# Performance work log

Measured on AMD Instinct MI355X. Metric: run time of the kernel, lower is better.

The kernel has to match this reference:

```python
import jax, jax.numpy as jnp
import numpy as np
from jax import lax

DIMS, IN_DIM, NW = 32, 32, 8
N, T, H, W = 8, 16, 112, 112
EPS = 1e-5

def setup_inputs() -> dict:
    key = jax.random.key(0)
    ks = jax.random.split(key, 12)
    fan = IN_DIM * 27
    inp = {
        'x': jax.random.normal(ks[0], (N, IN_DIM, T, H, W), jnp.float32),
        'std_x': jax.random.normal(ks[1], (N, 1, 32, 32), jnp.float32),
        'epochs_num': 5,
        'weights': jax.random.normal(ks[2], (NW, DIMS, IN_DIM, 3, 3, 3), jnp.float32) * np.sqrt(2.0 / fan),
        'biases': jax.random.normal(ks[3], (NW, DIMS), jnp.float32),
        'conv1_w': jax.random.normal(ks[4], (16, 1, 5, 5), jnp.float32) * 0.2,
        'conv1_b': jax.random.normal(ks[5], (16,), jnp.float32) * 0.1,
        'conv2_w': jax.random.normal(ks[6], (32, 16, 5, 5), jnp.float32) * 0.05,
        'conv2_b': jax.random.normal(ks[7], (32,), jnp.float32) * 0.1,
        'fc_w': jax.random.normal(ks[8], (NW, 32), jnp.float32) * 0.1,
        'fc_b': jax.random.normal(ks[9], (NW,), jnp.float32) * 0.1,
        'bn_gamma': jnp.ones((DIMS,), jnp.float32),
        'bn_beta': jnp.zeros((DIMS,), jnp.float32),
    }
    return inp

def _routing(std_x, c1w, c1b, c2w, c2b, fcw, fcb, tau):
    dn = ('NCHW', 'OIHW', 'NCHW')
    h = lax.conv_general_dilated(std_x, c1w, (1, 1), 'VALID', dimension_numbers=dn)
    h = jax.nn.relu(h + c1b[None, :, None, None])
    h = lax.conv_general_dilated(h, c2w, (1, 1), 'VALID', dimension_numbers=dn)
    h = jax.nn.relu(h + c2b[None, :, None, None])
    h = jnp.max(h, axis=(2, 3))                      # adaptive max pool to 1 -> [n,32]
    logits = h @ fcw.T + fcb                          # [n, num_weights]
    return jax.nn.softmax(logits / tau, axis=1)

def reference(x, std_x, epochs_num, weights, biases, conv1_w, conv1_b, conv2_w, conv2_b, fc_w, fc_b, bn_gamma, bn_beta):
    tau = 30.0 - 2.9 * epochs_num if epochs_num < 10 else 1.0
    phi = _routing(std_x, conv1_w, conv1_b, conv2_w, conv2_b, fc_w, fc_b, tau)
    dyn_w = jnp.einsum('bn,ncidhw->bcidhw', phi, weights)   # per-sample filters [n,dims,in,3,3,3]
    dyn_b = jnp.einsum('bn,nc->bc', phi, biases)            # [n,dims]
    dn3 = ('NCDHW', 'OIDHW', 'NCDHW')
    def per_sample(xi, wi):
        return lax.conv_general_dilated(xi[None], wi, (1, 1, 1), 'SAME', dimension_numbers=dn3)[0]
    y = jax.vmap(per_sample)(x, dyn_w)                      # [n,dims,T,H,W]
    y = y + dyn_b[:, :, None, None, None]
    # BatchNorm3d (training mode: batch stats, biased variance)
    mean = jnp.mean(y, axis=(0, 2, 3, 4))
    var = jnp.var(y, axis=(0, 2, 3, 4))
    y = (y - mean[None, :, None, None, None]) * lax.rsqrt(var + EPS)[None, :, None, None, None]
    y = y * bn_gamma[None, :, None, None, None] + bn_beta[None, :, None, None, None]
    return jax.nn.relu(y)
```

## Files before the change

### kernel.cpp

```cpp
#include <hip/hip_runtime.h>
#include <hip/hip_bf16.h>

#define IN_DIM 32
#define DIMS   32
#define NW     8
#define NB     8
#define TT     16
#define HH     112
#define WW     112
#define HW     (HH*WW)
#define CHW    (TT*HW)
#define EPS    1e-5f

typedef __attribute__((ext_vector_type(8))) short bf16x8;
typedef __attribute__((ext_vector_type(4))) float f32x4;

static __device__ __forceinline__ unsigned short f2bf(float f) {
    unsigned u = __float_as_uint(f);
    unsigned r = u + 0x7FFFu + ((u >> 16) & 1u);
    return (unsigned short)(r >> 16);
}

static __device__ __forceinline__ void gload_lds16(const void* gptr, void* lptr) {
    __builtin_amdgcn_global_load_lds(
        (const __attribute__((address_space(1))) unsigned int*)gptr,
        (__attribute__((address_space(3))) unsigned int*)lptr,
        16, 0, 0);
}

#define WSF_PHI    0
#define WSF_DYNB   64
#define WSF_STATS  320
#define WSF_ZERO   384
#define WSF_HDR_FLOATS 448
#define XT_USHORTS  ((size_t)NB*CHW*32)
#define WS_NEED_BYTES (WSF_HDR_FLOATS*4 + (size_t)NB*27*1024*2 + XT_USHORTS*2)

#define WS_PHI    0
#define WS_DYNW   64
#define WS_DYNB   221248
#define WS_STATS  221504
#define WS_SS     221568

__global__ __launch_bounds__(256)
void routing_conv1_kernel(const float* __restrict__ std_x,
                          const float* __restrict__ c1w, const float* __restrict__ c1b,
                          float* __restrict__ h1g)
{
    const int oc = blockIdx.x, b = blockIdx.y;
    const int tid = threadIdx.x;
    __shared__ float sx[1024];
    for (int i = tid; i < 1024; i += 256) sx[i] = std_x[b * 1024 + i];
    __syncthreads();

    float wloc[25];
    #pragma unroll
    for (int k = 0; k < 25; ++k) wloc[k] = c1w[oc * 25 + k];
    const float bias = c1b[oc];

    for (int idx = tid; idx < 784; idx += 256) {
        int xw = idx % 28, xh = idx / 28;
        float s = bias;
        #pragma unroll
        for (int ky = 0; ky < 5; ++ky)
            #pragma unroll
            for (int kx = 0; kx < 5; ++kx)
                s = fmaf(sx[(xh + ky) * 32 + xw + kx], wloc[ky * 5 + kx], s);
        h1g[(b * 16 + oc) * 784 + idx] = fmaxf(s, 0.f);
    }
}

__global__ __launch_bounds__(256)
void routing_conv2max_kernel(const float* __restrict__ h1g,
                             const float* __restrict__ c2w, const float* __restrict__ c2b,
                             float* __restrict__ cmax)
{
    const int oc = blockIdx.x, b = blockIdx.y;
    const int tid = threadIdx.x;
    __shared__ float h1s[16 * 784];
    __shared__ float wred[4];

    for (int i = tid; i < 16 * 784; i += 256) h1s[i] = h1g[b * (16 * 784) + i];
    __syncthreads();

    float m = 0.f;
    for (int idx = tid; idx < 576; idx += 256) {
        int xw = idx % 24, xh = idx / 24;
        float s = c2b[oc];
        for (int ic = 0; ic < 16; ++ic) {
            const float* hp = &h1s[ic * 784];
            const float* wp = &c2w[(oc * 16 + ic) * 25];
            #pragma unroll
            for (int ky = 0; ky < 5; ++ky)
                #pragma unroll
                for (int kx = 0; kx < 5; ++kx)
                    s = fmaf(hp[(xh + ky) * 28 + xw + kx], wp[ky * 5 + kx], s);
        }
        m = fmaxf(m, s);
    }
    #pragma unroll
    for (int off = 32; off >= 1; off >>= 1) m = fmaxf(m, __shfl_down(m, off));
    if ((tid & 63) == 0) wred[tid >> 6] = m;
    __syncthreads();
    if (tid == 0) {
        float r = fmaxf(fmaxf(wred[0], wred[1]), fmaxf(wred[2], wred[3]));
        cmax[b * 32 + oc] = r;
    }
}

__global__ __launch_bounds__(64)
void routing_fc_kernel(const float* __restrict__ cmax, const int* __restrict__ epochs,
                       const float* __restrict__ fcw, const float* __restrict__ fcb,
                       float* __restrict__ phi_out)
{
    const int tid = threadIdx.x;
    const int b = tid >> 3, n = tid & 7;
    int ep = epochs[0];
    float tau = (ep < 10) ? (30.0f - 2.9f * (float)ep) : 1.0f;
    float s = fcb[n];
    #pragma unroll
    for (int k = 0; k < 32; ++k) s = fmaf(cmax[b * 32 + k], fcw[n * 32 + k], s);
    s /= tau;
    float mx = s;
    #pragma unroll
    for (int off = 1; off < 8; off <<= 1) mx = fmaxf(mx, __shfl_xor(mx, off, 8));
    float e = expf(s - mx);
    float den = e;
    #pragma unroll
    for (int off = 1; off < 8; off <<= 1) den += __shfl_xor(den, off, 8);
    phi_out[b * 8 + n] = e / den;
}

#define XS 232
__global__ __launch_bounds__(256)
void xpose_kernel(const float* __restrict__ x, unsigned short* __restrict__ xT)
{
    const int h = blockIdx.x, t = blockIdx.y, b = blockIdx.z;
    const int tid = threadIdx.x;
    __shared__ __align__(16) unsigned char lds[32 * XS];

    for (int idx = tid; idx < 32 * 28; idx += 256) {
        int ic = idx / 28;
        int w4 = idx - ic * 28;
        const float4 v = *(const float4*)(x + (((size_t)(b * 32 + ic) * TT + t) * HW) + h * 112 + w4 * 4);
        uint2 pk;
        pk.x = (unsigned)f2bf(v.x) | ((unsigned)f2bf(v.y) << 16);
        pk.y = (unsigned)f2bf(v.z) | ((unsigned)f2bf(v.w) << 16);
        *(uint2*)(lds + ic * XS + w4 * 8) = pk;
    }
    __syncthreads();

    unsigned short* op = xT + ((((size_t)b * TT + t) * HH + h) * WW) * 32;
    for (int idx = tid; idx < 448; idx += 256) {
        int w = idx >> 2, icg = idx & 3;
        unsigned int pk[4];
        #pragma unroll
        for (int j = 0; j < 4; ++j) {
            unsigned short lo = *(unsigned short*)(lds + (icg * 8 + 2 * j) * XS + w * 2);
            unsigned short hi = *(unsigned short*)(lds + (icg * 8 + 2 * j + 1) * XS + w * 2);
            pk[j] = (unsigned int)lo | ((unsigned int)hi << 16);
        }
        uint4 v; v.x = pk[0]; v.y = pk[1]; v.z = pk[2]; v.w = pk[3];
        *(uint4*)(op + (size_t)w * 32 + icg * 8) = v;
    }
}

__global__ __launch_bounds__(256)
void dynwb_kernel(const float* __restrict__ phi, const float* __restrict__ weights,
                  const float* __restrict__ biases, unsigned short* __restrict__ dwb,
                  float* __restrict__ dyn_b, float* __restrict__ statszero)
{
    const int oc = blockIdx.x;
    const int b  = blockIdx.y;
    const int tid = threadIdx.x;
    __shared__ float ph[8];
    if (tid < 8) ph[tid] = phi[b * 8 + tid];
    __syncthreads();

    for (int i = tid; i < 864; i += 256) {
        float s = 0.f;
        #pragma unroll
        for (int n = 0; n < 8; ++n)
            s = fmaf(ph[n], weights[(size_t)(n * 32 + oc) * 864 + i], s);
        int ic = i / 27;
        int tap = i - 27 * ic;
        dwb[((size_t)(b * 27 + tap) << 10) + (oc << 5) + ic] = f2bf(s);
    }
    if (tid == 0) {
        float s = 0.f;
        #pragma unroll
        for (int n = 0; n < 8; ++n) s = fmaf(ph[n], biases[n * 32 + oc], s);
        dyn_b[b * 32 + oc] = s;
    }
    if (oc == 0 && b == 0 && tid < 128) statszero[tid] = 0.f;
}

#define XROWSTRIDE   1152
#define XLDS_BYTES   20736
#define WLDS_BYTES   55296
#define PLANE_BYTES_G 802816ull
__global__ __launch_bounds__(256, 2)
void convmf_kernel(const unsigned short* __restrict__ xT, const unsigned short* __restrict__ dwb,
                   const float* __restrict__ dyn_b, float* __restrict__ y,
                   float* __restrict__ stats)
{
    const int hblk = blockIdx.x / 7, wblk = blockIdx.x % 7;
    const int tpair = blockIdx.y, b = blockIdx.z;
    const int h0 = hblk * 16, w0 = wblk * 16, t0 = tpair * 2;
    const int tid = threadIdx.x;
    const int lane = tid & 63, wv = tid >> 6;
    const int l15 = lane & 15, lg = lane >> 4;

    __shared__ __align__(16) unsigned char wlds[WLDS_BYTES];
    __shared__ __align__(16) unsigned char xlds[XLDS_BYTES];
    __shared__ float sred[4][64];

    {
        const unsigned short* wb = dwb + (size_t)b * 27 * 1024;
        unsigned char* ldsw = wlds + (size_t)(tid & ~63) * 16;
        #pragma unroll
        for (int k = 0; k < 14; ++k) {
            if (k < 13 || tid < 128) {
                int cid = k * 256 + tid;
                int tap = cid >> 7;
                int rem = cid & 127;
                int oc  = rem >> 2;
                int icg_s = rem & 3;
                int icg_l = icg_s ^ ((oc >> 1) & 3);
                gload_lds16(wb + tap * 1024 + oc * 32 + icg_l * 8, ldsw + k * 4096);
            }
        }
    }

    const unsigned char* xbase = (const unsigned char*)xT + (size_t)b * TT * PLANE_BYTES_G;
    int srcoff[6], dsto[6];
    bool okj[6], valid[6];
    #pragma unroll
    for (int j = 0; j < 6; ++j) {
        int cid = j * 256 + tid;
        int hr = cid / 72, rem = cid - hr * 72;
        int p = rem >> 2, icg = rem & 3;
        int gh = h0 - 1 + hr, gw = w0 - 1 + p;
        valid[j] = (cid < 1296);
        okj[j] = valid[j] && ((unsigned)gh < (unsigned)HH) && ((unsigned)gw < (unsigned)WW);
        srcoff[j] = (gh * WW + gw) * 64 + icg * 16;
        dsto[j] = (hr * 72 + p * 4 + (icg ^ ((p >> 1) & 3))) * 16;
    }
    uint4 xs[6];

#define LOADX(TX) do {                                                        \
        const int tx_ = (TX);                                                 \
        const bool tok_ = ((unsigned)tx_ < (unsigned)TT);                     \
        const unsigned char* pb_ = xbase + (size_t)tx_ * PLANE_BYTES_G;       \
        _Pragma("unroll")                                                     \
        for (int j = 0; j < 6; ++j) {                                         \
            uint4 v_; v_.x = 0; v_.y = 0; v_.z = 0; v_.w = 0;                 \
            if (tok_ && okj[j]) v_ = *(const uint4*)(pb_ + srcoff[j]);        \
            xs[j] = v_;                                                       \
        }                                                                     \
    } while (0)

#define WRITEX() do {                                                         \
        _Pragma("unroll")                                                     \
        for (int j = 0; j < 6; ++j)                                           \
            if (valid[j]) *(uint4*)(xlds + dsto[j]) = xs[j];                  \
    } while (0)

    const int wsw = l15 * 64 + ((lg ^ ((l15 >> 1) & 3)) * 16);
    int xoff[3];
    #pragma unroll
    for (int dw = 0; dw < 3; ++dw) {
        int px = l15 + dw;
        xoff[dw] = px * 64 + ((lg ^ ((px >> 1) & 3)) * 16);
    }

    f32x4 acc0[4][2], acc1[4][2];
    #pragma unroll
    for (int g = 0; g < 4; ++g)
        #pragma unroll
        for (int M = 0; M < 2; ++M) { acc0[g][M] = (f32x4)0.f; acc1[g][M] = (f32x4)0.f; }

    LOADX(t0 - 1);
    asm volatile("s_waitcnt vmcnt(0)" ::: "memory");
    WRITEX();
    __syncthreads();

    #pragma unroll
    for (int tp = 0; tp < 4; ++tp) {
        if (tp < 3) LOADX(t0 + tp);

        const bool do0 = (tp <= 2), do1 = (tp >= 1);
        #pragma unroll
        for (int dhw = 0; dhw < 9; ++dhw) {
            const int dh = dhw / 3, dw = dhw - dh * 3;
            bf16x8 a00, a01, a10, a11;
            if (do0) {
                const int off = (tp * 9 + dhw) * 2048 + wsw;
                a00 = *(const bf16x8*)(wlds + off);
                a01 = *(const bf16x8*)(wlds + off + 1024);
            }
            if (do1) {
                const int off = ((tp - 1) * 9 + dhw) * 2048 + wsw;
                a10 = *(const bf16x8*)(wlds + off);
                a11 = *(const bf16x8*)(wlds + off + 1024);
            }
            const int rb = wv * 4 + dh;
            #pragma unroll
            for (int g = 0; g < 4; ++g) {
                bf16x8 bb = *(const bf16x8*)(xlds + (rb + g) * XROWSTRIDE + xoff[dw]);
                if (do0) {
                    acc0[g][0] = __builtin_amdgcn_mfma_f32_16x16x32_bf16(a00, bb, acc0[g][0], 0, 0, 0);
                    acc0[g][1] = __builtin_amdgcn_mfma_f32_16x16x32_bf16(a01, bb, acc0[g][1], 0, 0, 0);
                }
                if (do1) {
                    acc1[g][0] = __builtin_amdgcn_mfma_f32_16x16x32_bf16(a10, bb, acc1[g][0], 0, 0, 0);
                    acc1[g][1] = __builtin_amdgcn_mfma_f32_16x16x32_bf16(a11, bb, acc1[g][1], 0, 0, 0);
                }
            }
        }

        if (tp < 3) {
            __syncthreads();
            asm volatile("s_waitcnt vmcnt(0)" ::: "memory");
            WRITEX();
            __syncthreads();
        }
    }
#undef LOADX
#undef WRITEX

    f32x4 bias[2];
    #pragma unroll
    for (int M = 0; M < 2; ++M)
        #pragma unroll
        for (int r = 0; r < 4; ++r)
            bias[M][r] = dyn_b[b * 32 + 16 * M + lg * 4 + r];

    float sumv[2][4], sqv[2][4];
    #pragma unroll
    for (int M = 0; M < 2; ++M)
        #pragma unroll
        for (int r = 0; r < 4; ++r) { sumv[M][r] = 0.f; sqv[M][r] = 0.f; }

    #pragma unroll
    for (int g = 0; g < 4; ++g) {
        const int h = h0 + wv * 4 + g;
        #pragma unroll
        for (int M = 0; M < 2; ++M) {
            f32x4 v0 = acc0[g][M] + bias[M];
            f32x4 v1 = acc1[g][M] + bias[M];
            const int oc0 = 16 * M + lg * 4;
            size_t base = (((size_t)(b * 32 + oc0) * TT + t0) * HW) + h * 112 + w0 + l15;
            #pragma unroll
            for (int r = 0; r < 4; ++r) {
                sumv[M][r] += v0[r] + v1[r];
                sqv[M][r]  += v0[r] * v0[r] + v1[r] * v1[r];
                y[base + (size_t)r * TT * HW] = v0[r];
                y[base + (size_t)r * TT * HW + HW] = v1[r];
            }
        }
    }

    #pragma unroll
    for (int off = 1; off < 16; off <<= 1) {
        #pragma unroll
        for (int M = 0; M < 2; ++M)
            #pragma unroll
            for (int r = 0; r < 4; ++r) {
                sumv[M][r] += __shfl_xor(sumv[M][r], off);
                sqv[M][r]  += __shfl_xor(sqv[M][r], off);
            }
    }
    if (l15 == 0) {
        #pragma unroll
        for (int M = 0; M < 2; ++M)
            #pragma unroll
            for (int r = 0; r < 4; ++r) {
                int ch = 16 * M + lg * 4 + r;
                sred[wv][ch] = sumv[M][r];
                sred[wv][32 + ch] = sqv[M][r];
            }
    }
    __syncthreads();
    if (tid < 64) {
        float v = sred[0][tid] + sred[1][tid] + sred[2][tid] + sred[3][tid];
        atomicAdd(&stats[tid], v);
    }
}

__global__ __launch_bounds__(256)
void norm_relu_fused_kernel(float* __restrict__ y, const float* __restrict__ stats,
                            const float* __restrict__ gamma, const float* __restrict__ beta)
{
    __shared__ float ssc[32], ssh[32];
    if (threadIdx.x < 32) {
        int c = threadIdx.x;
        const float M = (float)NB * (float)CHW;
        float mean = stats[c] / M;
        float var  = stats[32 + c] / M - mean * mean;
        float sc = gamma[c] * rsqrtf(var + EPS);
        ssc[c] = sc;
        ssh[c] = beta[c] - mean * sc;
    }
    __syncthreads();

    const long long total4 = (long long)NB * DIMS * CHW / 4;
    const int nthreads = gridDim.x * blockDim.x;
    float4* y4 = reinterpret_cast<float4*>(y);
    for (long long i = (long long)blockIdx.x * blockDim.x + threadIdx.x; i < total4; i += nthreads) {
        int c = (int)((i / (CHW / 4)) & 31);
        float sc = ssc[c];
        float sh = ssh[c];
        float4 v = y4[i];
        v.x = fmaxf(fmaf(v.x, sc, sh), 0.f);
        v.y = fmaxf(fmaf(v.y, sc, sh), 0.f);
        v.z = fmaxf(fmaf(v.z, sc, sh), 0.f);
        v.w = fmaxf(fmaf(v.w, sc, sh), 0.f);
        y4[i] = v;
    }
}

__global__ __launch_bounds__(256)
void routing_kernel(const float* __restrict__ std_x, const int* __restrict__ epochs,
                    const float* __restrict__ c1w, const float* __restrict__ c1b,
                    const float* __restrict__ c2w, const float* __restrict__ c2b,
                    const float* __restrict__ fcw, const float* __restrict__ fcb,
                    float* __restrict__ phi_out)
{
    const int b = blockIdx.x;
    const int tid = threadIdx.x;
    __shared__ float sx[32 * 32];
    __shared__ float h1[16 * 28 * 28];
    __shared__ float cmax[32];

    for (int i = tid; i < 1024; i += 256) sx[i] = std_x[b * 1024 + i];
    if (tid < 32) cmax[tid] = 0.f;
    __syncthreads();

    for (int idx = tid; idx < 16 * 28 * 28; idx += 256) {
        int xw = idx % 28;
        int r = idx / 28;
        int xh = r % 28;
        int oc = r / 28;
        float s = c1b[oc];
        #pragma unroll
        for (int ky = 0; ky < 5; ++ky)
            #pragma unroll
            for (int kx = 0; kx < 5; ++kx)
                s = fmaf(sx[(xh + ky) * 32 + xw + kx], c1w[oc * 25 + ky * 5 + kx], s);
        h1[idx] = fmaxf(s, 0.f);
    }
    __syncthreads();

    for (int idx = tid; idx < 32 * 24 * 24; idx += 256) {
        int xw = idx % 24;
        int r = idx / 24;
        int xh = r % 24;
        int oc = r / 24;
        float s = c2b[oc];
        for (int ic = 0; ic < 16; ++ic) {
            const float* hp = &h1[ic * 784];
            const float* wp = &c2w[(oc * 16 + ic) * 25];
            #pragma unroll
            for (int ky = 0; ky < 5; ++ky)
                #pragma unroll
                for (int kx = 0; kx < 5; ++kx)
                    s = fmaf(hp[(xh + ky) * 28 + xw + kx], wp[ky * 5 + kx], s);
        }
        s = fmaxf(s, 0.f);
        atomicMax(reinterpret_cast<int*>(&cmax[oc]), __float_as_int(s));
    }
    __syncthreads();

    if (tid == 0) {
        int ep = epochs[0];
        float tau = (ep < 10) ? (30.0f - 2.9f * (float)ep) : 1.0f;
        float lg[8];
        float mx = -1e30f;
        #pragma unroll
        for (int n = 0; n < 8; ++n) {
            float s = fcb[n];
            #pragma unroll
            for (int k = 0; k < 32; ++k) s = fmaf(cmax[k], fcw[n * 32 + k], s);
            lg[n] = s / tau;
            mx = fmaxf(mx, lg[n]);
        }
        float den = 0.f;
        #pragma unroll
        for (int n = 0; n < 8; ++n) { lg[n] = expf(lg[n] - mx); den += lg[n]; }
        #pragma unroll
        for (int n = 0; n < 8; ++n) phi_out[b * 8 + n] = lg[n] / den;
    }
}

__global__ __launch_bounds__(256)
void dynw_kernel(const float* __restrict__ phi, const float* __restrict__ weights,
                 const float* __restrict__ biases, float* __restrict__ dyn_w,
                 float* __restrict__ dyn_b, float* __restrict__ stats)
{
    const int b = blockIdx.x;
    const int tid = threadIdx.x;
    __shared__ float ph[8];
    if (tid < 8) ph[tid] = phi[b * 8 + tid];
    __syncthreads();

    for (int j = tid; j < DIMS * IN_DIM * 27; j += 256) {
        float s = 0.f;
        #pragma unroll
        for (int n = 0; n < 8; ++n) s = fmaf(ph[n], weights[n * (DIMS * IN_DIM * 27) + j], s);
        dyn_w[b * (DIMS * IN_DIM * 27) + j] = s;
    }
    if (tid < 32) {
        float s = 0.f;
        #pragma unroll
        for (int n = 0; n < 8; ++n) s = fmaf(ph[n], biases[n * 32 + tid], s);
        dyn_b[b * 32 + tid] = s;
    }
    if (b == 0 && tid < 64) stats[tid] = 0.f;
}

__global__ __launch_bounds__(256)
void conv3d_kernel(const float* __restrict__ x, const float* __restrict__ dyn_w,
                   const float* __restrict__ dyn_b, float* __restrict__ y,
                   float* __restrict__ stats)
{
    const int htile = blockIdx.x;
    const int t     = blockIdx.y;
    const int b     = blockIdx.z;
    const int tid   = threadIdx.x;
    const int w     = tid & 127;
    const int hh    = tid >> 7;
    const int h0    = htile * 2;

    __shared__ float tile[3][8][4][114];

    float acc[32];
    #pragma unroll
    for (int c = 0; c < 32; ++c) acc[c] = 0.f;

    const float* wb = dyn_w + b * (DIMS * IN_DIM * 27);
    const float* xb = x + (size_t)b * IN_DIM * CHW;

    for (int ic0 = 0; ic0 < 32; ic0 += 8) {
        __syncthreads();
        for (int idx = tid; idx < 3 * 8 * 4 * 114; idx += 256) {
            int w_ = idx % 114;
            int r  = idx / 114;
            int h_ = r & 3;
            int r2 = r >> 2;
            int i_ = r2 & 7;
            int dt_ = r2 >> 3;
            int gt = t + dt_ - 1;
            int gh = h0 - 1 + h_;
            int gw = w_ - 1;
            float v = 0.f;
            if ((unsigned)gt < (unsigned)TT && (unsigned)gh < (unsigned)HH && (unsigned)gw < (unsigned)WW)
                v = xb[(size_t)((ic0 + i_) * TT + gt) * HW + gh * WW + gw];
            tile[dt_][i_][h_][w_] = v;
        }
        __syncthreads();

        if (w < WW) {
            for (int i = 0; i < 8; ++i) {
                #pragma unroll
                for (int dt = 0; dt < 3; ++dt) {
                    float xv[9];
                    #pragma unroll
                    for (int dh = 0; dh < 3; ++dh)
                        #pragma unroll
                        for (int dw = 0; dw < 3; ++dw)
                            xv[dh * 3 + dw] = tile[dt][i][hh + dh][w + dw];
                    const float* wp = wb + (ic0 + i) * 27 + dt * 9;
                    #pragma unroll
                    for (int c = 0; c < 32; ++c) {
                        const float* wc = wp + c * 864;
                        #pragma unroll
                        for (int k = 0; k < 9; ++k)
                            acc[c] = fmaf(xv[k], wc[k], acc[c]);
                    }
                }
            }
        }
    }

    const float* db = dyn_b + b * 32;
    if (w < WW) {
        #pragma unroll
        for (int c = 0; c < 32; ++c) acc[c] += db[c];
    }

    __shared__ float ssum[32], ssq[32];
    if (tid < 32) { ssum[tid] = 0.f; ssq[tid] = 0.f; }
    __syncthreads();
    #pragma unroll
    for (int c = 0; c < 32; ++c) {
        float s = (w < WW) ? acc[c] : 0.f;
        float q = s * s;
        #pragma unroll
        for (int off = 32; off >= 1; off >>= 1) {
            s += __shfl_down(s, off);
            q += __shfl_down(q, off);
        }
        if ((tid & 63) == 0) { atomicAdd(&ssum[c], s); atomicAdd(&ssq[c], q); }
    }
    __syncthreads();
    if (tid < 32) {
        atomicAdd(&stats[tid], ssum[tid]);
        atomicAdd(&stats[32 + tid], ssq[tid]);
    }

    if (w < WW) {
        size_t base = ((size_t)(b * 32) * TT + t) * HW + (size_t)(h0 + hh) * WW + w;
        #pragma unroll
        for (int c = 0; c < 32; ++c)
            y[base + (size_t)c * CHW] = acc[c];
    }
}

__global__ void stats_finalize_kernel(const float* __restrict__ stats,
                                      const float* __restrict__ gamma,
                                      const float* __restrict__ beta,
                                      float* __restrict__ scaleshift)
{
    int c = threadIdx.x;
    const float M = (float)NB * (float)CHW;
    float mean = stats[c] / M;
    float var  = stats[32 + c] / M - mean * mean;
    float sc = gamma[c] * rsqrtf(var + EPS);
    scaleshift[c] = sc;
    scaleshift[32 + c] = beta[c] - mean * sc;
}

__global__ __launch_bounds__(256)
void norm_relu_kernel(float* __restrict__ y, const float* __restrict__ scaleshift)
{
    const long long total4 = (long long)NB * DIMS * CHW / 4;
    const int nthreads = gridDim.x * blockDim.x;
    float4* y4 = reinterpret_cast<float4*>(y);
    for (long long i = (long long)blockIdx.x * blockDim.x + threadIdx.x; i < total4; i += nthreads) {
        int c = (int)((i / (CHW / 4)) & 31);
        float sc = scaleshift[c];
        float sh = scaleshift[32 + c];
        float4 v = y4[i];
        v.x = fmaxf(fmaf(v.x, sc, sh), 0.f);
        v.y = fmaxf(fmaf(v.y, sc, sh), 0.f);
        v.z = fmaxf(fmaf(v.z, sc, sh), 0.f);
        v.w = fmaxf(fmaf(v.w, sc, sh), 0.f);
        y4[i] = v;
    }
}

extern "C" void kernel_launch(void* const* d_in, const int* in_sizes, int n_in,
                              void* d_out, int out_size, void* d_ws, size_t ws_size,
                              hipStream_t stream)
{
    const float* x      = (const float*)d_in[0];
    const float* std_x  = (const float*)d_in[1];
    const int*   epochs = (const int*)d_in[2];
    const float* weights= (const float*)d_in[3];
    const float* biases = (const float*)d_in[4];
    const float* c1w    = (const float*)d_in[5];
    const float* c1b    = (const float*)d_in[6];
    const float* c2w    = (const float*)d_in[7];
    const float* c2b    = (const float*)d_in[8];
    const float* fcw    = (const float*)d_in[9];
    const float* fcb    = (const float*)d_in[10];
    const float* gamma  = (const float*)d_in[11];
    const float* beta   = (const float*)d_in[12];

    float* out = (float*)d_out;
    float* ws  = (float*)d_ws;

    if (ws_size >= WS_NEED_BYTES) {
        float* phi   = ws + WSF_PHI;
        float* dyn_b = ws + WSF_DYNB;
        float* stats = ws + WSF_STATS;
        unsigned short* dwb = (unsigned short*)(ws + WSF_HDR_FLOATS);
        unsigned short* xT  = dwb + (size_t)NB * 27 * 1024;
        float* h1g  = (float*)xT;
        float* cmax = h1g + NB * 16 * 784;

        routing_conv1_kernel<<<dim3(16, NB), 256, 0, stream>>>(std_x, c1w, c1b, h1g);
        routing_conv2max_kernel<<<dim3(32, NB), 256, 0, stream>>>(h1g, c2w, c2b, cmax);
        routing_fc_kernel<<<1, 64, 0, stream>>>(cmax, epochs, fcw, fcb, phi);
        dynwb_kernel<<<dim3(32, NB), 256, 0, stream>>>(phi, weights, biases, dwb, dyn_b, stats);
        xpose_kernel<<<dim3(HH, TT, NB), 256, 0, stream>>>(x, xT);
        convmf_kernel<<<dim3(49, 8, NB), 256, 0, stream>>>(xT, dwb, dyn_b, out, stats);
        norm_relu_fused_kernel<<<2048, 256, 0, stream>>>(out, stats, gamma, beta);
    } else {
        float* phi   = ws + WS_PHI;
        float* dyn_w = ws + WS_DYNW;
        float* dyn_b = ws + WS_DYNB;
        float* stats = ws + WS_STATS;
        float* ss    = ws + WS_SS;

        routing_kernel<<<NB, 256, 0, stream>>>(std_x, epochs, c1w, c1b, c2w, c2b, fcw, fcb, phi);
        dynw_kernel<<<NB, 256, 0, stream>>>(phi, weights, biases, dyn_w, dyn_b, stats);
        conv3d_kernel<<<dim3(HH / 2, TT, NB), 256, 0, stream>>>(x, dyn_w, dyn_b, out, stats);
        stats_finalize_kernel<<<1, 32, 0, stream>>>(stats, gamma, beta, ss);
        norm_relu_kernel<<<2048, 256, 0, stream>>>(out, ss);
    }
}
```

Before: 571.0 us.

## Fuse bf16 transpose into conv load and store conv output as bf16

Drops the separate transpose kernel. The conv kernel now reads fp32 x directly with per-element gathers and converts to bf16 while writing it into a swizzled LDS tile. The conv output goes to a bf16 intermediate buffer, which the norm/ReLU kernel reads before writing the final fp32 output, so intermediate traffic is halved. In exchange the conv now does 41 scalar gathers per thread, which raises register pressure, and it accumulates BN stats in fp32 while normalising values rounded to bf16, which loses precision.

Result: slower. 729.7 us (+27.8%).

```diff
diff --git a/kernel.cpp b/kernel.cpp
--- a/kernel.cpp
+++ b/kernel.cpp
@@ -20,6 +20,9 @@
     unsigned r = u + 0x7FFFu + ((u >> 16) & 1u);
     return (unsigned short)(r >> 16);
 }
+static __device__ __forceinline__ float bf2f(unsigned short u) {
+    return __uint_as_float(((unsigned)u) << 16);
+}
 
 static __device__ __forceinline__ void gload_lds16(const void* gptr, void* lptr) {
     __builtin_amdgcn_global_load_lds(
@@ -33,8 +36,8 @@
 #define WSF_STATS  320
 #define WSF_ZERO   384
 #define WSF_HDR_FLOATS 448
-#define XT_USHORTS  ((size_t)NB*CHW*32)
-#define WS_NEED_BYTES (WSF_HDR_FLOATS*4 + (size_t)NB*27*1024*2 + XT_USHORTS*2)
+#define YB_USHORTS  ((size_t)NB*DIMS*CHW)
+#define WS_NEED_BYTES (WSF_HDR_FLOATS*4 + (size_t)NB*27*1024*2 + YB_USHORTS*2)
 
 #define WS_PHI    0
 #define WS_DYNW   64
@@ -131,40 +134,6 @@
     phi_out[b * 8 + n] = e / den;
 }
 
-#define XS 232
-__global__ __launch_bounds__(256)
-void xpose_kernel(const float* __restrict__ x, unsigned short* __restrict__ xT)
-{
-    const int h = blockIdx.x, t = blockIdx.y, b = blockIdx.z;
-    const int tid = threadIdx.x;
-    __shared__ __align__(16) unsigned char lds[32 * XS];
-
-    for (int idx = tid; idx < 32 * 28; idx += 256) {
-        int ic = idx / 28;
-        int w4 = idx - ic * 28;
-        const float4 v = *(const float4*)(x + (((size_t)(b * 32 + ic) * TT + t) * HW) + h * 112 + w4 * 4);
-        uint2 pk;
-        pk.x = (unsigned)f2bf(v.x) | ((unsigned)f2bf(v.y) << 16);
-        pk.y = (unsigned)f2bf(v.z) | ((unsigned)f2bf(v.w) << 16);
-        *(uint2*)(lds + ic * XS + w4 * 8) = pk;
-    }
-    __syncthreads();
-
-    unsigned short* op = xT + ((((size_t)b * TT + t) * HH + h) * WW) * 32;
-    for (int idx = tid; idx < 448; idx += 256) {
-        int w = idx >> 2, icg = idx & 3;
-        unsigned int pk[4];
-        #pragma unroll
-        for (int j = 0; j < 4; ++j) {
-            unsigned short lo = *(unsigned short*)(lds + (icg * 8 + 2 * j) * XS + w * 2);
-            unsigned short hi = *(unsigned short*)(lds + (icg * 8 + 2 * j + 1) * XS + w * 2);
-            pk[j] = (unsigned int)lo | ((unsigned int)hi << 16);
-        }
-        uint4 v; v.x = pk[0]; v.y = pk[1]; v.z = pk[2]; v.w = pk[3];
-        *(uint4*)(op + (size_t)w * 32 + icg * 8) = v;
-    }
-}
-
 __global__ __launch_bounds__(256)
 void dynwb_kernel(const float* __restrict__ phi, const float* __restrict__ weights,
                   const float* __restrict__ biases, unsigned short* __restrict__ dwb,
@@ -195,13 +164,14 @@
     if (oc == 0 && b == 0 && tid < 128) statszero[tid] = 0.f;
 }
 
-#define XROWSTRIDE   1152
-#define XLDS_BYTES   20736
-#define WLDS_BYTES   55296
-#define PLANE_BYTES_G 802816ull
+#define XSTRIDE_PX 80
+#define XSTRIDE_GH 1440
+#define XLDS_BYTES 25920
+#define WLDS_BYTES 55296
+#define NE 41
 __global__ __launch_bounds__(256, 2)
-void convmf_kernel(const unsigned short* __restrict__ xT, const unsigned short* __restrict__ dwb,
-                   const float* __restrict__ dyn_b, float* __restrict__ y,
+void convmf_kernel(const float* __restrict__ x, const unsigned short* __restrict__ dwb,
+                   const float* __restrict__ dyn_b, unsigned short* __restrict__ ybf,
                    float* __restrict__ stats)
 {
     const int hblk = blockIdx.x / 7, wblk = blockIdx.x % 7;
@@ -213,7 +183,6 @@
 
     __shared__ __align__(16) unsigned char wlds[WLDS_BYTES];
     __shared__ __align__(16) unsigned char xlds[XLDS_BYTES];
-    __shared__ float sred[4][64];
 
     {
         const unsigned short* wb = dwb + (size_t)b * 27 * 1024;
@@ -232,46 +201,58 @@
         }
     }
 
-    const unsigned char* xbase = (const unsigned char*)xT + (size_t)b * TT * PLANE_BYTES_G;
-    int srcoff[6], dsto[6];
-    bool okj[6], valid[6];
-    #pragma unroll
-    for (int j = 0; j < 6; ++j) {
-        int cid = j * 256 + tid;
-        int hr = cid / 72, rem = cid - hr * 72;
-        int p = rem >> 2, icg = rem & 3;
-        int gh = h0 - 1 + hr, gw = w0 - 1 + p;
-        valid[j] = (cid < 1296);
-        okj[j] = valid[j] && ((unsigned)gh < (unsigned)HH) && ((unsigned)gw < (unsigned)WW);
-        srcoff[j] = (gh * WW + gw) * 64 + icg * 16;
-        dsto[j] = (hr * 72 + p * 4 + (icg ^ ((p >> 1) & 3))) * 16;
-    }
-    uint4 xs[6];
+    int voff[NE];
+    unsigned long long okm = 0ull;
+    #pragma unroll
+    for (int k = 0; k < NE; ++k) {
+        int e = k * 256 + tid;
+        int row = e / 18;
+        int gw = e - row * 18;
+        int gh = row >> 5;
+        int ic = row & 31;
+        int ghg = h0 - 1 + gh;
+        int gwg = w0 - 1 + gw;
+        bool ok = (e < 10368) && ((unsigned)ghg < (unsigned)HH) && ((unsigned)gwg < (unsigned)WW);
+        voff[k] = ok ? (ic * CHW + ghg * WW + gwg) : 0;
+        if (ok) okm |= (1ull << k);
+    }
+    const float* xb = x + (size_t)b * 32 * CHW;
+
+    float xd[NE];
+    unsigned long long wmask = 0ull;
 
 #define LOADX(TX) do {                                                        \
         const int tx_ = (TX);                                                 \
-        const bool tok_ = ((unsigned)tx_ < (unsigned)TT);                     \
-        const unsigned char* pb_ = xbase + (size_t)tx_ * PLANE_BYTES_G;       \
+        wmask = ((unsigned)tx_ < (unsigned)TT) ? okm : 0ull;                  \
+        const int tcl_ = min(max(tx_, 0), TT - 1);                            \
+        const float* pb_ = xb + (size_t)tcl_ * HW;                            \
         _Pragma("unroll")                                                     \
-        for (int j = 0; j < 6; ++j) {                                         \
-            uint4 v_; v_.x = 0; v_.y = 0; v_.z = 0; v_.w = 0;                 \
-            if (tok_ && okj[j]) v_ = *(const uint4*)(pb_ + srcoff[j]);        \
-            xs[j] = v_;                                                       \
+        for (int k = 0; k < NE; ++k) xd[k] = pb_[voff[k]];                    \
+    } while (0)
+
+#define WRITEX() do {                                                         \
+        _Pragma("unroll")                                                     \
+        for (int k = 0; k < NE; ++k) {                                        \
+            int e_ = k * 256 + tid;                                           \
+            if (k < NE - 1 || e_ < 10368) {                                   \
+                int row_ = e_ / 18;                                           \
+                int gw_ = e_ - row_ * 18;                                     \
+                int gh_ = row_ >> 5;                                          \
+                int ic_ = row_ & 31;                                          \
+                int dst_ = gh_ * XSTRIDE_GH + gw_ * XSTRIDE_PX                \
+                         + (((ic_ >> 3) ^ (gw_ & 3)) << 4) + (ic_ & 7) * 2;   \
+                float v_ = ((wmask >> k) & 1ull) ? xd[k] : 0.f;               \
+                *(unsigned short*)(xlds + dst_) = f2bf(v_);                   \
+            }                                                                 \
         }                                                                     \
     } while (0)
 
-#define WRITEX() do {                                                         \
-        _Pragma("unroll")                                                     \
-        for (int j = 0; j < 6; ++j)                                           \
-            if (valid[j]) *(uint4*)(xlds + dsto[j]) = xs[j];                  \
-    } while (0)
-
     const int wsw = l15 * 64 + ((lg ^ ((l15 >> 1) & 3)) * 16);
     int xoff[3];
     #pragma unroll
     for (int dw = 0; dw < 3; ++dw) {
         int px = l15 + dw;
-        xoff[dw] = px * 64 + ((lg ^ ((px >> 1) & 3)) * 16);
+        xoff[dw] = px * XSTRIDE_PX + ((lg ^ (px & 3)) << 4);
     }
 
     f32x4 acc0[4][2], acc1[4][2];
@@ -307,7 +288,7 @@
             const int rb = wv * 4 + dh;
             #pragma unroll
             for (int g = 0; g < 4; ++g) {
-                bf16x8 bb = *(const bf16x8*)(xlds + (rb + g) * XROWSTRIDE + xoff[dw]);
+                bf16x8 bb = *(const bf16x8*)(xlds + (rb + g) * XSTRIDE_GH + xoff[dw]);
                 if (do0) {
                     acc0[g][0] = __builtin_amdgcn_mfma_f32_16x16x32_bf16(a00, bb, acc0[g][0], 0, 0, 0);
                     acc0[g][1] = __builtin_amdgcn_mfma_f32_16x16x32_bf16(a01, bb, acc0[g][1], 0, 0, 0);
@@ -329,6 +310,9 @@
 #undef LOADX
 #undef WRITEX
 
+    __syncthreads();
+    float (*sredp)[64] = (float(*)[64])xlds;
+
     f32x4 bias[2];
     #pragma unroll
     for (int M = 0; M < 2; ++M)
@@ -355,8 +339,8 @@
             for (int r = 0; r < 4; ++r) {
                 sumv[M][r] += v0[r] + v1[r];
                 sqv[M][r]  += v0[r] * v0[r] + v1[r] * v1[r];
-                y[base + (size_t)r * TT * HW] = v0[r];
-                y[base + (size_t)r * TT * HW + HW] = v1[r];
+                ybf[base + (size_t)r * CHW] = f2bf(v0[r]);
+                ybf[base + (size_t)r * CHW + HW] = f2bf(v1[r]);
             }
         }
     }
@@ -377,19 +361,20 @@
             #pragma unroll
             for (int r = 0; r < 4; ++r) {
                 int ch = 16 * M + lg * 4 + r;
-                sred[wv][ch] = sumv[M][r];
-                sred[wv][32 + ch] = sqv[M][r];
+                sredp[wv][ch] = sumv[M][r];
+                sredp[wv][32 + ch] = sqv[M][r];
             }
     }
     __syncthreads();
     if (tid < 64) {
-        float v = sred[0][tid] + sred[1][tid] + sred[2][tid] + sred[3][tid];
+        float v = sredp[0][tid] + sredp[1][tid] + sredp[2][tid] + sredp[3][tid];
         atomicAdd(&stats[tid], v);
     }
 }
 
 __global__ __launch_bounds__(256)
-void norm_relu_fused_kernel(float* __restrict__ y, const float* __restrict__ stats,
+void norm_relu_fused_kernel(const unsigned short* __restrict__ ybf, float* __restrict__ out,
+                            const float* __restrict__ stats,
                             const float* __restrict__ gamma, const float* __restrict__ beta)
 {
     __shared__ float ssc[32], ssh[32];
@@ -404,19 +389,26 @@
     }
     __syncthreads();
 
-    const long long total4 = (long long)NB * DIMS * CHW / 4;
+    const long long total8 = (long long)NB * DIMS * CHW / 8;
     const int nthreads = gridDim.x * blockDim.x;
-    float4* y4 = reinterpret_cast<float4*>(y);
-    for (long long i = (long long)blockIdx.x * blockDim.x + threadIdx.x; i < total4; i += nthreads) {
-        int c = (int)((i / (CHW / 4)) & 31);
+    const uint4* y8 = reinterpret_cast<const uint4*>(ybf);
+    for (long long i = (long long)blockIdx.x * blockDim.x + threadIdx.x; i < total8; i += nthreads) {
+        int c = (int)((i / (CHW / 8)) & 31);
         float sc = ssc[c];
         float sh = ssh[c];
-        float4 v = y4[i];
-        v.x = fmaxf(fmaf(v.x, sc, sh), 0.f);
-        v.y = fmaxf(fmaf(v.y, sc, sh), 0.f);
-        v.z = fmaxf(fmaf(v.z, sc, sh), 0.f);
-        v.w = fmaxf(fmaf(v.w, sc, sh), 0.f);
-        y4[i] = v;
+        uint4 v = y8[i];
+        float4 o0, o1;
+        o0.x = fmaxf(fmaf(bf2f((unsigned short)(v.x & 0xffff)), sc, sh), 0.f);
+        o0.y = fmaxf(fmaf(bf2f((unsigned short)(v.x >> 16)),    sc, sh), 0.f);
+        o0.z = fmaxf(fmaf(bf2f((unsigned short)(v.y & 0xffff)), sc, sh), 0.f);
+        o0.w = fmaxf(fmaf(bf2f((unsigned short)(v.y >> 16)),    sc, sh), 0.f);
+        o1.x = fmaxf(fmaf(bf2f((unsigned short)(v.z & 0xffff)), sc, sh), 0.f);
+        o1.y = fmaxf(fmaf(bf2f((unsigned short)(v.z >> 16)),    sc, sh), 0.f);
+        o1.z = fmaxf(fmaf(bf2f((unsigned short)(v.w & 0xffff)), sc, sh), 0.f);
+        o1.w = fmaxf(fmaf(bf2f((unsigned short)(v.w >> 16)),    sc, sh), 0.f);
+        float4* op = reinterpret_cast<float4*>(out + (size_t)i * 8);
+        op[0] = o0;
+        op[1] = o1;
     }
 }
 
@@ -676,17 +668,16 @@
         float* dyn_b = ws + WSF_DYNB;
         float* stats = ws + WSF_STATS;
         unsigned short* dwb = (unsigned short*)(ws + WSF_HDR_FLOATS);
-        unsigned short* xT  = dwb + (size_t)NB * 27 * 1024;
-        float* h1g  = (float*)xT;
+        unsigned short* ybf = dwb + (size_t)NB * 27 * 1024;
+        float* h1g  = (float*)ybf;
         float* cmax = h1g + NB * 16 * 784;
 
         routing_conv1_kernel<<<dim3(16, NB), 256, 0, stream>>>(std_x, c1w, c1b, h1g);
         routing_conv2max_kernel<<<dim3(32, NB), 256, 0, stream>>>(h1g, c2w, c2b, cmax);
         routing_fc_kernel<<<1, 64, 0, stream>>>(cmax, epochs, fcw, fcb, phi);
         dynwb_kernel<<<dim3(32, NB), 256, 0, stream>>>(phi, weights, biases, dwb, dyn_b, stats);
-        xpose_kernel<<<dim3(HH, TT, NB), 256, 0, stream>>>(x, xT);
-        convmf_kernel<<<dim3(49, 8, NB), 256, 0, stream>>>(xT, dwb, dyn_b, out, stats);
-        norm_relu_fused_kernel<<<2048, 256, 0, stream>>>(out, stats, gamma, beta);
+        convmf_kernel<<<dim3(49, 8, NB), 256, 0, stream>>>(x, dwb, dyn_b, ybf, stats);
+        norm_relu_fused_kernel<<<2048, 256, 0, stream>>>(ybf, out, stats, gamma, beta);
     } else {
         float* phi   = ws + WS_PHI;
         float* dyn_w = ws + WS_DYNW;
```
